# Optimization experiments

Hardware: AMD Instinct MI355X
Metric: run time of the kernel (lower is better)

## Reference

```python
import math
import jax, jax.numpy as jnp
import numpy as np

GRAIN = 300   # bilinear / grain dim (gpconv output channels)
PAD = 4       # explicit zero padding before each conv1d / conv2d
POOL = 40     # adaptive pool target (mf_model_pool_dim)

def conv1d_k2(x, w, b):
    # x: [B, L, Cin], w: [Cout, Cin, 2] -> [B, L-1, Cout]
    return (jnp.einsum('blc,oc->blo', x[:, :-1], w[:, :, 0])
            + jnp.einsum('blc,oc->blo', x[:, 1:], w[:, :, 1]) + b)

def kmax_last(x, k):
    # torch-style k-max pooling: top-k values along last axis, original order kept
    idx = jnp.sort(jax.lax.top_k(x, k)[1], axis=-1)
    return jnp.take_along_axis(x, idx, axis=-1)

def kmax_len(x, k):
    # k-max pooling over the length axis (axis=1) of [B, L, C]
    return jnp.swapaxes(kmax_last(jnp.swapaxes(x, 1, 2), k), 1, 2)

def adaptive_max_1d(x, out, axis):
    # torch AdaptiveMaxPool semantics along one axis; windows precomputed statically
    L = x.shape[axis]
    r = np.arange(out)
    starts = (r * L) // out
    ends = -((-(r + 1) * L) // out)
    maxw = int((ends - starts).max())
    off = starts[:, None] + np.arange(maxw)[None, :]
    mask = jnp.asarray(off < ends[:, None])
    idxs = np.minimum(off, L - 1)
    xm = jnp.moveaxis(x, axis, -1)
    g = jnp.where(mask, xm[..., idxs], -jnp.inf)
    return jnp.moveaxis(g.max(-1), -1, axis)

def conv2d_p4(x, w, b):
    y = jax.lax.conv_general_dilated(x, w, (1, 1), [(PAD, PAD), (PAD, PAD)],
                                     dimension_numbers=('NCHW', 'OIHW', 'NCHW'))
    return y + b[None, :, None, None]

def gp_tower(x, w1, b1, w2, b2, w3, b3, k1, k2):
    # multigranular conv tower: zero-pad(4) -> conv1d(k=2) -> tanh -> k-max pool
    g0 = kmax_last(x, GRAIN)                      # [B, L, 300]
    def block(z, w, b, k):
        z = jnp.pad(z, ((0, 0), (PAD, PAD), (0, 0)))
        return kmax_len(jnp.tanh(conv1d_k2(z, w, b)), k)
    p1 = block(x, w1, b1, k1)                     # [B, k1, 300]
    p2 = block(p1, w2, b2, k2)                    # [B, k2, 300]
    p3 = block(p2, w3, b3, 1)                     # [B, 1, 300]
    return jnp.concatenate([g0, p1, p2, p3], axis=1)

def _forward(query, pos_doc, neg_docs, qw1, qb1, qw2, qb2, qw3, qb3,
             dw1, db1, dw2, db2, dw3, db3, bw, bb,
             mw1, mb1, mw2, mb2, mw3, mb3, lw, lb):
    B, Lq, _ = query.shape
    S, _, Ld, _ = neg_docs.shape
    kq1, kq2 = max(4, math.ceil(2 * Lq / 3)), max(4, math.ceil(Lq / 3))
    kd1, kd2 = max(4, math.ceil(2 * Ld / 3)), max(4, math.ceil(Ld / 3))
    qg = gp_tower(query, qw1, qb1, qw2, qb2, qw3, qb3, kq1, kq2)   # [B, Nq, 300]
    docs = jnp.concatenate([pos_doc[None], neg_docs], 0).reshape((S + 1) * B, Ld, -1)
    dg = gp_tower(docs, dw1, db1, dw2, db2, dw3, db3, kd1, kd2)    # [(S+1)B, Nd, 300]
    Nq, Nd = qg.shape[1], dg.shape[1]
    dg = dg.reshape(S + 1, B, Nd, GRAIN)
    # batched bilinear matching + sigmoid (replaces the O(Nq*Nd) per-pair loop)
    qt = jnp.einsum('bqd,de->bqe', qg, bw)
    M = jax.nn.sigmoid(jnp.einsum('bqe,sbje->sbqj', qt, dg) + bb[0])
    M = M.reshape((S + 1) * B, Nq, Nd)
    x = adaptive_max_1d(adaptive_max_1d(M, POOL, 1), POOL, 2)[:, None]  # [N,1,40,40]
    for w, b in ((mw1, mb1), (mw2, mb2), (mw3, mb3)):
        x = jax.nn.sigmoid(conv2d_p4(x, w, b))
        x = adaptive_max_1d(adaptive_max_1d(x, POOL, 2), POOL, 3)
        x = x.max(axis=1, keepdims=True)          # k-max(k=1) over channels
    feat = x[:, 0]                                # [N, 40, 40]
    h = jax.nn.sigmoid(jnp.einsum('nij,j->ni', feat, lw[0]) + lb[0])
    s = jax.nn.sigmoid(h @ lw[0] + lb[0])
    return s.reshape(S + 1, B)                    # row 0 = pos-doc scores

def setup_inputs():
    ks = jax.random.split(jax.random.key(0), 26)
    def n(i, shape, s=0.05):
        return jax.random.normal(ks[i], shape, dtype=jnp.float32) * s
    return dict(
        query=jax.random.normal(ks[0], (16, 239, 1024), dtype=jnp.float32),
        pos_doc=jax.random.normal(ks[1], (16, 479, 1024), dtype=jnp.float32),
        neg_docs=jax.random.normal(ks[2], (4, 16, 479, 1024), dtype=jnp.float32),
        qw1=n(3, (300, 1024, 2)), qb1=n(4, (300,)),
        qw2=n(5, (300, 300, 2)), qb2=n(6, (300,)),
        qw3=n(7, (300, 300, 2)), qb3=n(8, (300,)),
        dw1=n(9, (300, 1024, 2)), db1=n(10, (300,)),
        dw2=n(11, (300, 300, 2)), db2=n(12, (300,)),
        dw3=n(13, (300, 300, 2)), db3=n(14, (300,)),
        bw=n(15, (300, 300)), bb=n(16, (1,)),
        mw1=n(17, (50, 1, 2, 2)), mb1=n(18, (50,)),
        mw2=n(19, (50, 1, 2, 2)), mb2=n(20, (50,)),
        mw3=n(21, (50, 1, 2, 2)), mb3=n(22, (50,)),
        lw=n(23, (1, 40)), lb=n(24, (1,)),
    )

def reference(query, pos_doc, neg_docs, qw1, qb1, qw2, qb2, qw3, qb3,
              dw1, db1, dw2, db2, dw3, db3, bw, bb,
              mw1, mb1, mw2, mb2, mw3, mb3, lw, lb):
    return _forward(query, pos_doc, neg_docs, qw1, qb1, qw2, qb2, qw3, qb3,
                    dw1, db1, dw2, db2, dw3, db3, bw, bb,
                    mw1, mb1, mw2, mb2, mw3, mb3, lw, lb)
```

## Files before the change

kernel.cpp:

```cpp
#include <hip/hip_runtime.h>
#include <hip/hip_bf16.h>
#include <math.h>

typedef unsigned long long ull;
typedef unsigned int uint;
typedef unsigned short ushort_t;

typedef short bf16x8 __attribute__((ext_vector_type(8)));
typedef float floatx4 __attribute__((ext_vector_type(4)));

__device__ inline ushort_t f2b(float f) {
    uint u = __float_as_uint(f);
    u = u + 0x7fffu + ((u >> 16) & 1u);
    return (ushort_t)(u >> 16);
}

__device__ inline uint kmap16(ushort_t u) {
    return (u & 0x8000u) ? (uint)((~u) & 0xFFFFu) : (uint)(u | 0x8000u);
}
__device__ inline ushort_t kinv16(uint k) {
    return (k & 0x8000u) ? (ushort_t)(k ^ 0x8000u) : (ushort_t)((~k) & 0xFFFFu);
}

__device__ inline void async_copy16(const void* g, void* l) {
    __builtin_amdgcn_global_load_lds(
        (const __attribute__((address_space(1))) void*)g,
        (__attribute__((address_space(3))) void*)l, 16, 0, 0);
}

__global__ void prep_w2_kernel(const float* __restrict__ w, ushort_t* __restrict__ Wb,
                               int C, int CP) {
    int CHn = CP / 32;
    int total = CHn * 2 * 20 * 512;
    for (int i = blockIdx.x * blockDim.x + threadIdx.x; i < total;
         i += gridDim.x * blockDim.x) {
        int e = i & 7;
        int lane = (i >> 3) & 63;
        int rest = i >> 9;
        int g = rest % 20;
        int tc = rest / 20;
        int t = tc & 1, c = tc >> 1;
        int o = g * 16 + (lane & 15);
        int ch = c * 32 + (lane >> 4) * 8 + e;
        float v = (o < 300 && ch < C) ? w[((size_t)o * C + ch) * 2 + t] : 0.f;
        Wb[i] = f2b(v);
    }
}

__global__ void prep_bw_kernel(const float* __restrict__ bw, ushort_t* __restrict__ bwb) {
    int i = blockIdx.x * 256 + threadIdx.x;
    if (i >= 320 * 320) return;
    int e = i / 320, d = i - e * 320;
    bwb[i] = (e < 300 && d < 300) ? f2b(bw[d * 300 + e]) : (ushort_t)0;
}

__global__ __launch_bounds__(256) void x_pad_bf16_kernel(
    const float* __restrict__ src, const float* __restrict__ src2, int split_n,
    long long s_nstr, int Lin, ushort_t* __restrict__ dst, int rows)
{
    int r = blockIdx.x, n = blockIdx.y;
    const float* sp = (split_n > 0 && n >= split_n)
                          ? src2 + (size_t)(n - split_n) * s_nstr
                          : src + (size_t)n * s_nstr;
    int g = r - 4;
    ushort_t* dp = dst + ((size_t)n * rows + r) * 1024;
    int c = threadIdx.x * 4;
    ushort4 o = {0, 0, 0, 0};
    if (g >= 0 && g < Lin) {
        float4 v = *(const float4*)&sp[(size_t)g * 1024 + c];
        o.x = f2b(v.x); o.y = f2b(v.y); o.z = f2b(v.z); o.w = f2b(v.w);
    }
    *(ushort4*)&dp[c] = o;
}

template <int CP>
__global__ __launch_bounds__(256, 2) void conv_wave_kernel(
    const ushort_t* __restrict__ xq, long long xq_nstr,
    const ushort_t* __restrict__ xd, long long xd_nstr,
    const ushort_t* __restrict__ Wq, const ushort_t* __restrict__ Wd,
    const float* __restrict__ bq, const float* __restrict__ bd,
    int Lout_q, int Lout_d, int mtiles_q, int mtiles_d,
    ushort_t* __restrict__ yt)
{
    constexpr int CH = CP / 32;
    constexpr int SLOT = 129 * 64;
    __shared__ char Abuf[4][2][SLOT];

    int tid = threadIdx.x, wid = tid >> 6, lane = tid & 63;
    int u = blockIdx.x * 4 + wid;
    int md5 = mtiles_d * 5, DOCU = md5 * 80;

    const ushort_t* x; const ushort_t* W; const float* bias;
    int Lout, mt, nt, ng;
    if (u < DOCU) {
        int nd = u / md5, r = u - nd * md5;
        mt = r / 5; nt = r - mt * 5;
        x = xd + (size_t)nd * xd_nstr; W = Wd; bias = bd; Lout = Lout_d;
        ng = 16 + nd;
    } else {
        int v = u - DOCU, mq5 = mtiles_q * 5;
        int nq = v / mq5, r = v - nq * mq5;
        mt = r / 5; nt = r - mt * 5;
        x = xq + (size_t)nq * xq_nstr; W = Wq; bias = bq; Lout = Lout_q;
        ng = nq;
    }
    int l0 = mt * 128;
    int lrow = lane & 15, quad = lane >> 4;

    const ushort_t* gMain = x + (size_t)(l0 + (lane >> 2)) * CP
                              + ((lane & 3) ^ ((lane >> 3) & 3)) * 8;
    const ushort_t* gXtra = x + (size_t)(l0 + 128) * CP + lane * 8;

    const ushort_t* Bw = W + (size_t)(nt * 4) * 512 + lane * 8;

    int baseA[2];
#pragma unroll
    for (int t = 0; t < 2; t++) {
        int rr = lrow + t;
        baseA[t] = rr * 64 + ((quad ^ ((rr >> 1) & 3)) << 4);
    }

    floatx4 acc[8][4];
#pragma unroll
    for (int i = 0; i < 8; i++)
#pragma unroll
        for (int j = 0; j < 4; j++) acc[i][j] = (floatx4){0.f, 0.f, 0.f, 0.f};

    char* lb0 = &Abuf[wid][0][0];

    auto STAGE = [&](int cc, int slot) {
        char* lb = lb0 + slot * SLOT;
        const ushort_t* gs = gMain + cc * 32;
#pragma unroll
        for (int g = 0; g < 8; g++)
            async_copy16(gs + (size_t)(g * 16) * CP, lb + g * 1024);
        if (lane < 4) async_copy16(gXtra + cc * 32, lb + 8192);
    };
    auto LOADB = [&](bf16x8 (&bf)[2][4], int cc) {
#pragma unroll
        for (int t = 0; t < 2; t++)
#pragma unroll
            for (int ns = 0; ns < 4; ns++)
                bf[t][ns] = *(const bf16x8*)(Bw + (size_t)((cc * 2 + t) * 20 + ns) * 512);
    };
    auto COMPUTE = [&](bf16x8 (&bf)[2][4], int slot) {
        const char* ab = lb0 + slot * SLOT;
        __builtin_amdgcn_s_setprio(1);
#pragma unroll
        for (int t = 0; t < 2; t++) {
#pragma unroll
            for (int ms = 0; ms < 8; ms++) {
                bf16x8 af = *(const bf16x8*)(ab + baseA[t] + ms * 1024);
#pragma unroll
                for (int ns = 0; ns < 4; ns++)
                    acc[ms][ns] = __builtin_amdgcn_mfma_f32_16x16x32_bf16(
                        af, bf[t][ns], acc[ms][ns], 0, 0, 0);
            }
        }
        __builtin_amdgcn_s_setprio(0);
    };
    auto WAITA = [&]() {
        asm volatile("s_waitcnt vmcnt(8)" ::: "memory");
        __builtin_amdgcn_sched_barrier(0);
    };

    bf16x8 bA[2][4], bB[2][4];

    STAGE(0, 0);
    __builtin_amdgcn_sched_barrier(0x38F);
    LOADB(bA, 0);

    for (int c = 0; c < CH; c += 2) {
        WAITA();
        if (c + 1 < CH) {
            STAGE(c + 1, (c + 1) & 1);
            __builtin_amdgcn_sched_barrier(0x38F);
            LOADB(bB, c + 1);
            __builtin_amdgcn_sched_barrier(0x38F);
        }
        COMPUTE(bA, c & 1);

        WAITA();
        if (c + 2 < CH) {
            STAGE(c + 2, (c + 2) & 1);
            __builtin_amdgcn_sched_barrier(0x38F);
            LOADB(bA, c + 2);
            __builtin_amdgcn_sched_barrier(0x38F);
        }
        COMPUTE(bB, (c + 1) & 1);
    }

    ushort_t* yp = yt + (size_t)ng * (320 * 488);
#pragma unroll
    for (int ns = 0; ns < 4; ns++) {
        int o = nt * 64 + ns * 16 + lrow;
        if (o >= 300) continue;
        float bo = bias[o];
        ushort_t* orow = yp + (size_t)o * 488;
#pragma unroll
        for (int ms = 0; ms < 8; ms++) {
            int l = l0 + ms * 16 + quad * 4;
            if (l + 3 < Lout) {
                ushort4 v;
                v.x = f2b(tanhf(acc[ms][ns][0] + bo));
                v.y = f2b(tanhf(acc[ms][ns][1] + bo));
                v.z = f2b(tanhf(acc[ms][ns][2] + bo));
                v.w = f2b(tanhf(acc[ms][ns][3] + bo));
                *(ushort4*)&orow[l] = v;
            } else {
#pragma unroll
                for (int r = 0; r < 4; r++)
                    if (l + r < Lout) orow[l + r] = f2b(tanhf(acc[ms][ns][r] + bo));
            }
        }
    }
}

__global__ __launch_bounds__(256) void topk_g0_kernel(
    const ushort_t* __restrict__ src, int CC, long long s_n,
    ushort_t* __restrict__ out, long long o_n, long long o_c)
{
    __shared__ uint hist[4][257];

    int tid = threadIdx.x, wid = tid >> 6, lane = tid & 63;
    int row = blockIdx.x * 4 + wid;
    int n = row / CC, c = row - n * CC;
    const ushort_t* sp = src + (size_t)n * s_n + (size_t)c * 1024;

    const uint* sp32 = (const uint*)(sp + (size_t)lane * 16);
    uint pk[8];
    {
        uint4 va = *(const uint4*)sp32;
        uint4 vb = *(const uint4*)(sp32 + 4);
        pk[0] = va.x; pk[1] = va.y; pk[2] = va.z; pk[3] = va.w;
        pk[4] = vb.x; pk[5] = vb.y; pk[6] = vb.z; pk[7] = vb.w;
    }
    uint key[16];
#pragma unroll
    for (int i = 0; i < 8; i++) {
        uint w = pk[i];
        uint s = w & 0x80008000u;
        w ^= 0x80008000u | ((s >> 15) * 0x7fffu);
        key[2 * i] = w & 0xffffu;
        key[2 * i + 1] = w >> 16;
    }

    uint* hg = hist[wid];
    uint rem = 300, bsel = 0, T = 0;

#pragma unroll
    for (int round = 0; round < 2; round++) {
#pragma unroll
        for (int t = 0; t < 4; t++) hg[lane + t * 64] = 0;
        __builtin_amdgcn_sched_barrier(0);
        if (round == 0) {
#pragma unroll
            for (int e = 0; e < 16; e++) atomicAdd(&hg[key[e] >> 8], 1u);
        } else {
#pragma unroll
            for (int e = 0; e < 16; e++)
                if ((key[e] >> 8) == bsel) atomicAdd(&hg[key[e] & 255u], 1u);
        }
        __builtin_amdgcn_sched_barrier(0);
        uint hv[4], Sr = 0;
#pragma unroll
        for (int t = 0; t < 4; t++) { hv[t] = hg[lane * 4 + t]; Sr += hv[t]; }
        uint suf = Sr;
#pragma unroll
        for (int off = 1; off < 64; off <<= 1) {
            uint u = __shfl_down(suf, off);
            if (lane + off < 64) suf += u;
        }
        uint acc = suf - Sr;
        uint found = 0;
#pragma unroll
        for (int t = 3; t >= 0; t--) {
            uint h = hv[t];
            if (!found && acc < rem && acc + h >= rem)
                found = ((uint)(lane * 4 + t) << 16) | (rem - acc);
            acc += h;
        }
#pragma unroll
        for (int off = 1; off < 64; off <<= 1) found |= __shfl_xor(found, off);
        if (round == 0) {
            bsel = found >> 16;
            rem = found & 0xffffu;
        } else {
            T = (bsel << 8) | (found >> 16);
            rem = found & 0xffffu;
        }
        __builtin_amdgcn_sched_barrier(0);
    }

    uint gtc = 0, eqc = 0;
#pragma unroll
    for (int e = 0; e < 16; e++) {
        gtc += (key[e] > T) ? 1u : 0u;
        eqc += (key[e] == T) ? 1u : 0u;
    }
    uint pack = (gtc << 16) | eqc, incl = pack;
#pragma unroll
    for (int off = 1; off < 64; off <<= 1) {
        uint u = __shfl_up(incl, off);
        if (lane >= off) incl += u;
    }
    uint excl = incl - pack;
    uint gt_b = excl >> 16, eq_b = excl & 0xffffu;

    ushort_t* dp = out + (size_t)n * o_n + (size_t)c * o_c;
#pragma unroll
    for (int e = 0; e < 16; e++) {
        uint kk = key[e];
        if (kk > T) {
            uint pos = gt_b + (eq_b < rem ? eq_b : rem);
            dp[pos] = kinv16(kk);
            gt_b++;
        } else if (kk == T) {
            if (eq_b < rem) dp[gt_b + eq_b] = kinv16(kk);
            eq_b++;
        }
    }
}

__global__ __launch_bounds__(256) void topk_cols_kernel(
    const ushort_t* __restrict__ yt2,
    int Lq, int Ld, int kq, int kd,
    ushort_t* __restrict__ qg, int qoff,
    ushort_t* __restrict__ dg, int doff,
    ushort_t* __restrict__ pq, long long pq_nstr,
    ushort_t* __restrict__ pd, long long pd_nstr)
{
    __shared__ __align__(16) ushort_t xin[32][488];
    __shared__ __align__(16) uint hist[32 * 257];
    ushort_t* otile = (ushort_t*)hist;

    int cg = blockIdx.x, n = blockIdx.y;
    int c0 = cg * 32;
    bool isq = (n < 16);
    int L = isq ? Lq : Ld;
    int k = isq ? kq : kd;
    int nd = isq ? n : n - 16;
    int tid = threadIdx.x;

    const ushort_t* src = yt2 + (size_t)n * (320 * 488) + (size_t)c0 * 488;
    for (int i = tid; i < 32 * 61; i += 256) {
        int j = i / 61, s = i - j * 61;
        *(uint4*)&xin[j][s * 8] = *(const uint4*)&src[(size_t)j * 488 + s * 8];
    }
    __syncthreads();

    int g = tid >> 3, r = tid & 7;
    uint* hg = &hist[g * 257];
    bool cval = (c0 + g) < 300;
    int S = (L + 7) >> 3;
    int llo = r * S, lhi = llo + S;
    if (lhi > L) lhi = L;
    if (llo > L) llo = L;

    uint rem = (uint)k;
    uint bsel = 0;
    uint Tt = 0;

#pragma unroll
    for (int round = 0; round < 2; round++) {
        for (int t = r; t < 256; t += 8) hg[t] = 0;
        for (int l = llo; l < lhi; l++) {
            uint key = cval ? kmap16(xin[g][l]) : 0x8000u;
            if (round == 0)
                atomicAdd(&hg[key >> 8], 1u);
            else if ((key >> 8) == bsel)
                atomicAdd(&hg[key & 255u], 1u);
        }
        uint hv[32];
        uint Sr = 0;
        int b0 = r * 32;
#pragma unroll
        for (int t = 0; t < 32; t++) { hv[t] = hg[b0 + t]; Sr += hv[t]; }
        uint suf = Sr;
#pragma unroll
        for (int off = 1; off < 8; off <<= 1) {
            uint u = __shfl_down(suf, off);
            if (r + off < 8) suf += u;
        }
        uint acc = suf - Sr;
        uint found = 0;
#pragma unroll
        for (int t = 31; t >= 0; t--) {
            uint h = hv[t];
            if (!found && acc < rem && acc + h >= rem)
                found = ((uint)(b0 + t) << 16) | (rem - acc);
            acc += h;
        }
#pragma unroll
        for (int off = 1; off < 8; off <<= 1) found |= __shfl_xor(found, off);
        if (round == 0) {
            bsel = found >> 16;
            rem = found & 0xffffu;
        } else {
            Tt = (bsel << 8) | (found >> 16);
            rem = found & 0xffffu;
        }
    }

    uint gtc = 0, eqc = 0;
    for (int l = llo; l < lhi; l++) {
        uint key = cval ? kmap16(xin[g][l]) : 0x8000u;
        gtc += (key > Tt) ? 1u : 0u;
        eqc += (key == Tt) ? 1u : 0u;
    }
    uint pack = (gtc << 16) | eqc, incl = pack;
#pragma unroll
    for (int off = 1; off < 8; off <<= 1) {
        uint u = __shfl_up(incl, off);
        if (r >= off) incl += u;
    }
    uint excl = incl - pack;
    uint gt_b = excl >> 16, eq_b = excl & 0xffffu;

    __syncthreads();

    for (int l = llo; l < lhi; l++) {
        uint key = cval ? kmap16(xin[g][l]) : 0x8000u;
        if (key > Tt) {
            uint pos = gt_b + (eq_b < rem ? eq_b : rem);
            otile[pos * 32 + g] = kinv16(key);
            gt_b++;
        } else if (key == Tt) {
            if (eq_b < rem) otile[(gt_b + eq_b) * 32 + g] = kinv16(key);
            eq_b++;
        }
    }
    __syncthreads();

    ushort_t* d1 = isq ? qg + ((size_t)nd * 480 + qoff) * 320 + c0
                       : dg + ((size_t)nd * 960 + doff) * 320 + c0;
    ushort_t* d2 = 0;
    if (isq) { if (pq) d2 = pq + (size_t)nd * pq_nstr + 4 * 320 + c0; }
    else     { if (pd) d2 = pd + (size_t)nd * pd_nstr + 4 * 320 + c0; }

    for (int i = tid; i < k * 8; i += 256) {
        int p = i >> 3, s = i & 7;
        ushort4 v = *(ushort4*)&otile[p * 32 + s * 4];
        *(ushort4*)&d1[(size_t)p * 320 + s * 4] = v;
        if (d2) *(ushort4*)&d2[(size_t)p * 320 + s * 4] = v;
    }
}

__global__ __launch_bounds__(256) void qt_mfma_kernel(
    const ushort_t* __restrict__ qgb, const ushort_t* __restrict__ bwb,
    ushort_t* __restrict__ qtb)
{
    int mt = blockIdx.x, b = blockIdx.y;
    int tid = threadIdx.x, wid = tid >> 6, lane = tid & 63;
    int wn = wid * 80, lrow = lane & 15, quad = lane >> 4;

    const ushort_t* A = qgb + ((size_t)b * 480 + mt * 48 + lrow) * 320 + quad * 8;
    const ushort_t* B = bwb + (size_t)(wn + lrow) * 320 + quad * 8;

    floatx4 acc[3][5];
#pragma unroll
    for (int i = 0; i < 3; i++)
#pragma unroll
        for (int j = 0; j < 5; j++) acc[i][j] = (floatx4){0.f, 0.f, 0.f, 0.f};

#pragma unroll 5
    for (int c0 = 0; c0 < 320; c0 += 32) {
        bf16x8 af[3], bfr[5];
#pragma unroll
        for (int ms = 0; ms < 3; ms++)
            af[ms] = *(const bf16x8*)&A[(size_t)(ms * 16) * 320 + c0];
#pragma unroll
        for (int ns = 0; ns < 5; ns++)
            bfr[ns] = *(const bf16x8*)&B[(size_t)(ns * 16) * 320 + c0];
#pragma unroll
        for (int ms = 0; ms < 3; ms++)
#pragma unroll
            for (int ns = 0; ns < 5; ns++)
                acc[ms][ns] = __builtin_amdgcn_mfma_f32_16x16x32_bf16(
                    af[ms], bfr[ns], acc[ms][ns], 0, 0, 0);
    }

    ushort_t* out = qtb + ((size_t)b * 480 + mt * 48) * 320;
#pragma unroll
    for (int ms = 0; ms < 3; ms++)
#pragma unroll
        for (int ns = 0; ns < 5; ns++)
#pragma unroll
            for (int r = 0; r < 4; r++)
                out[(size_t)(ms * 16 + quad * 4 + r) * 320 + wn + ns * 16 + lrow] =
                    f2b(acc[ms][ns][r]);
}

__global__ __launch_bounds__(256) void mpool_mfma_kernel(
    const ushort_t* __restrict__ qtb16, const ushort_t* __restrict__ dgb16,
    const float* __restrict__ bb, float* __restrict__ mp)
{
    __shared__ float pool[2 * 12 * 192];

    int jb = blockIdx.x;
    int qb = blockIdx.y;
    int n  = blockIdx.z;
    int b  = n & 15;

    int tid = threadIdx.x;
    int wid = tid >> 6, lane = tid & 63;
    int wm2 = wid >> 1;
    int wm = wm2 * 48, wn = (wid & 1) * 96;
    int lrow = lane & 15, quad = lane >> 4;

    const ushort_t* Abase = qtb16 + ((size_t)b * 480 + qb * 96 + wm) * 320 + quad * 8;
    const ushort_t* Bbase = dgb16 + ((size_t)n * 960 + jb * 192 + wn) * 320 + quad * 8;

    floatx4 acc[3][6];
#pragma unroll
    for (int i = 0; i < 3; i++)
#pragma unroll
        for (int j = 0; j < 6; j++) acc[i][j] = (floatx4){0.f, 0.f, 0.f, 0.f};

#pragma unroll 2
    for (int c0 = 0; c0 < 320; c0 += 32) {
        bf16x8 af[3], bfr[6];
#pragma unroll
        for (int mt = 0; mt < 3; mt++)
            af[mt] = *(const bf16x8*)&Abase[(size_t)(mt * 16 + lrow) * 320 + c0];
#pragma unroll
        for (int nt = 0; nt < 6; nt++)
            bfr[nt] = *(const bf16x8*)&Bbase[(size_t)(nt * 16 + lrow) * 320 + c0];
#pragma unroll
        for (int mt = 0; mt < 3; mt++)
#pragma unroll
            for (int nt = 0; nt < 6; nt++)
                acc[mt][nt] = __builtin_amdgcn_mfma_f32_16x16x32_bf16(
                    af[mt], bfr[nt], acc[mt][nt], 0, 0, 0);
    }

#pragma unroll
    for (int mt = 0; mt < 3; mt++) {
        int g = mt * 4 + quad;
#pragma unroll
        for (int nt = 0; nt < 6; nt++) {
            floatx4 a = acc[mt][nt];
            float rm = fmaxf(fmaxf(a[0], a[1]), fmaxf(a[2], a[3]));
            pool[(wm2 * 12 + g) * 192 + wn + nt * 16 + lrow] = rm;
        }
    }
    __syncthreads();

    if (tid < 64) {
        int qw = tid >> 3, jw = tid & 7;
        int slab = qw >> 2, w = qw & 3;
        float m = -INFINITY;
        const float* pp = &pool[(slab * 12 + w * 3) * 192 + jw * 24];
        for (int g = 0; g < 3; g++)
            for (int cc = 0; cc < 24; cc++)
                m = fmaxf(m, pp[g * 192 + cc]);
        float sig = 1.f / (1.f + expf(-(m + bb[0])));
        mp[(size_t)n * 1600 + (size_t)(qb * 8 + qw) * 40 + (jb * 8 + jw)] = sig;
    }
}

#define OCG 10
__global__ __launch_bounds__(256) void convblock_atomic_kernel(
    const float* __restrict__ X, const float* __restrict__ w,
    const float* __restrict__ bias, uint* __restrict__ Y)
{
    __shared__ float xp[48 * 48];
    __shared__ float ys[47 * 47];
    __shared__ float t1[40 * 47];
    __shared__ float outacc[1600];

    int n = blockIdx.x, t = threadIdx.x;
    int oc0 = blockIdx.y * OCG;
    const float* xn = X + (size_t)n * 1600;
    for (int i = t; i < 48 * 48; i += 256) {
        int r = i / 48, c = i - r * 48;
        int rr = r - 4, cc = c - 4;
        xp[i] = (rr >= 0 && rr < 40 && cc >= 0 && cc < 40) ? xn[rr * 40 + cc] : 0.f;
    }
    for (int i = t; i < 1600; i += 256) outacc[i] = 0.f;
    __syncthreads();

    for (int oc = oc0; oc < oc0 + OCG; oc++) {
        float w00 = w[oc * 4 + 0], w01 = w[oc * 4 + 1];
        float w10 = w[oc * 4 + 2], w11 = w[oc * 4 + 3];
        float bo = bias[oc];
        for (int i = t; i < 47 * 47; i += 256) {
            int r = i / 47, c = i - r * 47;
            float v = xp[r * 48 + c] * w00 + xp[r * 48 + c + 1] * w01
                    + xp[(r + 1) * 48 + c] * w10 + xp[(r + 1) * 48 + c + 1] * w11 + bo;
            ys[i] = 1.f / (1.f + expf(-v));
        }
        __syncthreads();
        for (int i = t; i < 40 * 47; i += 256) {
            int r = i / 47, c = i - r * 47;
            int s = (47 * r) / 40, e = (47 * (r + 1) + 39) / 40;
            float m = ys[s * 47 + c];
            for (int x = s + 1; x < e; x++) m = fmaxf(m, ys[x * 47 + c]);
            t1[i] = m;
        }
        __syncthreads();
        for (int i = t; i < 1600; i += 256) {
            int r = i / 40, c = i - r * 40;
            int s = (47 * c) / 40, e = (47 * (c + 1) + 39) / 40;
            float m = t1[r * 47 + s];
            for (int x = s + 1; x < e; x++) m = fmaxf(m, t1[r * 47 + x]);
            outacc[i] = fmaxf(outacc[i], m);
        }
        __syncthreads();
    }
    for (int i = t; i < 1600; i += 256)
        atomicMax(&Y[(size_t)n * 1600 + i], __float_as_uint(outacc[i]));
}

__global__ __launch_bounds__(64) void head_kernel(
    const float* __restrict__ feat, const float* __restrict__ lw,
    const float* __restrict__ lb, float* __restrict__ out)
{
    __shared__ float hs[40];
    int n = blockIdx.x, t = threadIdx.x;
    const float* f = feat + (size_t)n * 1600;
    if (t < 40) {
        float a = 0.f;
        for (int j = 0; j < 40; j++) a += f[t * 40 + j] * lw[j];
        hs[t] = 1.f / (1.f + expf(-(a + lb[0])));
    }
    __syncthreads();
    if (t == 0) {
        float a = 0.f;
        for (int i = 0; i < 40; i++) a += hs[i] * lw[i];
        out[n] = 1.f / (1.f + expf(-(a + lb[0])));
    }
}

extern "C" void kernel_launch(void* const* d_in, const int* in_sizes, int n_in,
                              void* d_out, int out_size, void* d_ws, size_t ws_size,
                              hipStream_t stream) {
    const float* query    = (const float*)d_in[0];
    const float* pos_doc  = (const float*)d_in[1];
    const float* neg_docs = (const float*)d_in[2];
    const float* qw1 = (const float*)d_in[3];  const float* qb1 = (const float*)d_in[4];
    const float* qw2 = (const float*)d_in[5];  const float* qb2 = (const float*)d_in[6];
    const float* qw3 = (const float*)d_in[7];  const float* qb3 = (const float*)d_in[8];
    const float* dw1 = (const float*)d_in[9];  const float* db1 = (const float*)d_in[10];
    const float* dw2 = (const float*)d_in[11]; const float* db2 = (const float*)d_in[12];
    const float* dw3 = (const float*)d_in[13]; const float* db3 = (const float*)d_in[14];
    const float* bw  = (const float*)d_in[15]; const float* bb  = (const float*)d_in[16];
    const float* mw1 = (const float*)d_in[17]; const float* mb1 = (const float*)d_in[18];
    const float* mw2 = (const float*)d_in[19]; const float* mb2 = (const float*)d_in[20];
    const float* mw3 = (const float*)d_in[21]; const float* mb3 = (const float*)d_in[22];
    const float* lw  = (const float*)d_in[23]; const float* lb  = (const float*)d_in[24];

    float* ws = (float*)d_ws;
    ushort_t* qw1b  = (ushort_t*)(ws + 0);
    ushort_t* qw2b  = (ushort_t*)(ws + 327680);
    ushort_t* qw3b  = (ushort_t*)(ws + 430080);
    ushort_t* dw1b  = (ushort_t*)(ws + 532480);
    ushort_t* dw2b  = (ushort_t*)(ws + 860160);
    ushort_t* dw3b  = (ushort_t*)(ws + 962560);
    ushort_t* bwb   = (ushort_t*)(ws + 1064960);
    ushort_t* qgb16 = (ushort_t*)(ws + 1116160);
    ushort_t* dgb16 = (ushort_t*)(ws + 2344960);
    ushort_t* yt    = (ushort_t*)(ws + 14632960);
    ushort_t* qxb   = (ushort_t*)(ws + 22128640);
    ushort_t* p1q   = (ushort_t*)(ws + 22128640);
    ushort_t* p2q   = (ushort_t*)(ws + 22640640);
    ushort_t* dxb   = (ushort_t*)(ws + 24291328);
    ushort_t* p1d   = (ushort_t*)(ws + 24291328);
    ushort_t* p2d   = (ushort_t*)(ws + 28899328);
    ushort_t* qtb16 = (ushort_t*)(ws + 31459328);
    float*    mp    = ws + 32688128;
    float*    ya    = ws + 32816128;
    float*    yb    = ws + 32944128;
    float*    yc    = ws + 33072128;

    prep_w2_kernel<<<1280, 256, 0, stream>>>(qw1, qw1b, 1024, 1024);
    prep_w2_kernel<<<400, 256, 0, stream>>>(qw2, qw2b, 300, 320);
    prep_w2_kernel<<<400, 256, 0, stream>>>(qw3, qw3b, 300, 320);
    prep_w2_kernel<<<1280, 256, 0, stream>>>(dw1, dw1b, 1024, 1024);
    prep_w2_kernel<<<400, 256, 0, stream>>>(dw2, dw2b, 300, 320);
    prep_w2_kernel<<<400, 256, 0, stream>>>(dw3, dw3b, 300, 320);
    prep_bw_kernel<<<400, 256, 0, stream>>>(bw, bwb);

    {
        dim3 g(264, 16);
        x_pad_bf16_kernel<<<g, 256, 0, stream>>>(query, nullptr, 0,
                                                 239LL * 1024, 239, qxb, 264);
    }
    {
        dim3 g(520, 80);
        x_pad_bf16_kernel<<<g, 256, 0, stream>>>(pos_doc, neg_docs, 16,
                                                 479LL * 1024, 479, dxb, 520);
    }

    topk_g0_kernel<<<(16 * 239) / 4, 256, 0, stream>>>(
        qxb + 4 * 1024, 239, 264LL * 1024, qgb16, 480LL * 320, 320);
    topk_g0_kernel<<<(80 * 479) / 4, 256, 0, stream>>>(
        dxb + 4 * 1024, 479, 520LL * 1024, dgb16, 960LL * 320, 320);

    conv_wave_kernel<1024><<<440, 256, 0, stream>>>(
        qxb, 264LL * 1024, dxb, 520LL * 1024,
        qw1b, dw1b, qb1, db1, 246, 486, 2, 4, yt);

    hipMemsetAsync(p1q, 0, 16 * 200 * 320 * 2, stream);
    hipMemsetAsync(p2q, 0, 16 * 104 * 320 * 2, stream);
    hipMemsetAsync(p1d, 0, (size_t)80 * 360 * 320 * 2, stream);
    hipMemsetAsync(p2d, 0, (size_t)80 * 200 * 320 * 2, stream);
    hipMemsetAsync(ya, 0, 80 * 1600 * 4, stream);
    hipMemsetAsync(yb, 0, 80 * 1600 * 4, stream);
    hipMemsetAsync(yc, 0, 80 * 1600 * 4, stream);

    {
        dim3 g(10, 96);
        topk_cols_kernel<<<g, 256, 0, stream>>>(
            yt, 246, 486, 160, 320,
            qgb16, 239, dgb16, 479,
            p1q, 200LL * 320, p1d, 360LL * 320);
    }

    conv_wave_kernel<320><<<340, 256, 0, stream>>>(
        p1q, 200LL * 320, p1d, 360LL * 320,
        qw2b, dw2b, qb2, db2, 167, 327, 2, 3, yt);

    {
        dim3 g(10, 96);
        topk_cols_kernel<<<g, 256, 0, stream>>>(
            yt, 167, 327, 80, 160,
            qgb16, 399, dgb16, 799,
            p2q, 104LL * 320, p2d, 200LL * 320);
    }

    conv_wave_kernel<320><<<220, 256, 0, stream>>>(
        p2q, 104LL * 320, p2d, 200LL * 320,
        qw3b, dw3b, qb3, db3, 87, 167, 1, 2, yt);

    {
        dim3 g(10, 96);
        topk_cols_kernel<<<g, 256, 0, stream>>>(
            yt, 87, 167, 1, 1,
            qgb16, 479, dgb16, 959,
            nullptr, 0, nullptr, 0);
    }

    {
        dim3 g(10, 16);
        qt_mfma_kernel<<<g, 256, 0, stream>>>(qgb16, bwb, qtb16);
    }
    {
        dim3 g(5, 5, 80);
        mpool_mfma_kernel<<<g, 256, 0, stream>>>(qtb16, dgb16, bb, mp);
    }

    {
        dim3 g(80, 5);
        convblock_atomic_kernel<<<g, 256, 0, stream>>>(mp, mw1, mb1, (uint*)ya);
        convblock_atomic_kernel<<<g, 256, 0, stream>>>(ya, mw2, mb2, (uint*)yb);
        convblock_atomic_kernel<<<g, 256, 0, stream>>>(yb, mw3, mb3, (uint*)yc);
    }
    head_kernel<<<80, 64, 0, stream>>>(yc, lw, lb, (float*)d_out);
}
```

Measured before the change: 1.112 ms.

## Add 64-row conv tile kernel with 3-stage pipeline for layers two and three

Adds a new conv kernel variant that computes 64-row M tiles per wave (instead of 128), uses a triple-buffered async LDS staging pipeline and allows 3 blocks per CU. Layers two and three now launch this variant with more tiles and blocks, while the original 128-row kernel is kept under a new name for the first layer. The aim is to raise parallelism and occupancy for the smaller later convolutions, which underfill the GPU. The cost is less reuse of each weight load across rows and more blocks to schedule.

After: 1.081 ms. 1.03x faster.

```diff
diff --git a/kernel.cpp b/kernel.cpp
--- a/kernel.cpp
+++ b/kernel.cpp
@@ -74,7 +74,137 @@
 }
 
 template <int CP>
-__global__ __launch_bounds__(256, 2) void conv_wave_kernel(
+__global__ __launch_bounds__(256, 3) void conv_wave_kernel(
+    const ushort_t* __restrict__ xq, long long xq_nstr,
+    const ushort_t* __restrict__ xd, long long xd_nstr,
+    const ushort_t* __restrict__ Wq, const ushort_t* __restrict__ Wd,
+    const float* __restrict__ bq, const float* __restrict__ bd,
+    int Lout_q, int Lout_d, int mtiles_q, int mtiles_d,
+    ushort_t* __restrict__ yt)
+{
+    constexpr int CH = CP / 32;
+    __shared__ char Abuf[4][3][4160];
+
+    int tid = threadIdx.x, wid = tid >> 6, lane = tid & 63;
+    int u = blockIdx.x * 4 + wid;
+    int md5 = mtiles_d * 5, DOCU = md5 * 80;
+
+    const ushort_t* x; const ushort_t* W; const float* bias;
+    int Lout, mt, nt, ng;
+    if (u < DOCU) {
+        int nd = u / md5, r = u - nd * md5;
+        mt = r / 5; nt = r - mt * 5;
+        x = xd + (size_t)nd * xd_nstr; W = Wd; bias = bd; Lout = Lout_d;
+        ng = 16 + nd;
+    } else {
+        int v = u - DOCU, mq5 = mtiles_q * 5;
+        int nq = v / mq5, r = v - nq * mq5;
+        mt = r / 5; nt = r - mt * 5;
+        x = xq + (size_t)nq * xq_nstr; W = Wq; bias = bq; Lout = Lout_q;
+        ng = nq;
+    }
+    int l0 = mt * 64;
+    int lrow = lane & 15, quad = lane >> 4;
+
+    const ushort_t* gMain = x + (size_t)(l0 + (lane >> 2)) * CP
+                              + ((lane & 3) ^ ((lane >> 3) & 3)) * 8;
+    const ushort_t* gXtra = x + (size_t)(l0 + 64) * CP + lane * 8;
+
+    const ushort_t* Bw = W + (size_t)(nt * 4) * 512 + lane * 8;
+
+    int offA[2][4];
+#pragma unroll
+    for (int t = 0; t < 2; t++)
+#pragma unroll
+        for (int ms = 0; ms < 4; ms++) {
+            int r = ms * 16 + lrow + t;
+            offA[t][ms] = r * 64 + ((quad ^ ((r >> 1) & 3)) << 4);
+        }
+
+    floatx4 acc[4][4];
+#pragma unroll
+    for (int i = 0; i < 4; i++)
+#pragma unroll
+        for (int j = 0; j < 4; j++) acc[i][j] = (floatx4){0.f, 0.f, 0.f, 0.f};
+
+    char* lb0 = &Abuf[wid][0][0];
+
+    auto STAGE = [&](int cc, int slot) {
+        char* lb = lb0 + slot * 4160;
+        const ushort_t* gs = gMain + cc * 32;
+        async_copy16(gs, lb);
+        async_copy16(gs + (size_t)16 * CP, lb + 1024);
+        async_copy16(gs + (size_t)32 * CP, lb + 2048);
+        async_copy16(gs + (size_t)48 * CP, lb + 3072);
+        if (lane < 4) async_copy16(gXtra + cc * 32, lb + 4096);
+    };
+
+    STAGE(0, 0);
+    STAGE(1, 1);
+
+    for (int c = 0; c < CH; c++) {
+        if (c == 0) asm volatile("s_waitcnt vmcnt(5)" ::: "memory");
+        else        asm volatile("s_waitcnt vmcnt(8)" ::: "memory");
+        __builtin_amdgcn_sched_barrier(0);
+
+        bf16x8 bf[2][4];
+#pragma unroll
+        for (int t = 0; t < 2; t++)
+#pragma unroll
+            for (int ns = 0; ns < 4; ns++)
+                bf[t][ns] = *(const bf16x8*)(Bw + (size_t)((c * 2 + t) * 20 + ns) * 512);
+        __builtin_amdgcn_sched_barrier(0x38F);
+
+        if (c + 2 < CH) STAGE(c + 2, (c + 2) % 3);
+
+        const char* ab = lb0 + (c % 3) * 4160;
+        __builtin_amdgcn_s_setprio(1);
+#pragma unroll
+        for (int t = 0; t < 2; t++) {
+            bf16x8 af[4];
+#pragma unroll
+            for (int ms = 0; ms < 4; ms++)
+                af[ms] = *(const bf16x8*)(ab + offA[t][ms]);
+#pragma unroll
+            for (int ms = 0; ms < 4; ms++)
+#pragma unroll
+                for (int ns = 0; ns < 4; ns++)
+                    acc[ms][ns] = __builtin_amdgcn_mfma_f32_16x16x32_bf16(
+                        af[ms], bf[t][ns], acc[ms][ns], 0, 0, 0);
+        }
+        __builtin_amdgcn_s_setprio(0);
+    }
+
+    ushort_t* yp = yt + (size_t)ng * (320 * 488);
+#pragma unroll
+    for (int ns = 0; ns < 4; ns++) {
+        int o = nt * 64 + ns * 16 + lrow;
+        if (o >= 300) continue;
+        float bo = bias[o];
+        ushort_t* orow = yp + (size_t)o * 488;
+#pragma unroll
+        for (int ms = 0; ms < 4; ms++) {
+            int l = l0 + ms * 16 + quad * 4;
+            if (l + 3 < Lout) {
+                ushort4 v;
+                v.x = f2b(tanhf(acc[ms][ns][0] + bo));
+                v.y = f2b(tanhf(acc[ms][ns][1] + bo));
+                v.z = f2b(tanhf(acc[ms][ns][2] + bo));
+                v.w = f2b(tanhf(acc[ms][ns][3] + bo));
+                *(ushort4*)&orow[l] = v;
+            } else {
+#pragma unroll
+                for (int r = 0; r < 4; r++)
+                    if (l + r < Lout) orow[l + r] = f2b(tanhf(acc[ms][ns][r] + bo));
+            }
+        }
+    }
+}
+
+template <int CP>
+__global__ __launch_bounds__(256)
+__attribute__((amdgpu_waves_per_eu(2, 2)))
+void conv_wave128_kernel(
     const ushort_t* __restrict__ xq, long long xq_nstr,
     const ushort_t* __restrict__ xd, long long xd_nstr,
     const ushort_t* __restrict__ Wq, const ushort_t* __restrict__ Wd,
@@ -697,7 +827,7 @@
     topk_g0_kernel<<<(80 * 479) / 4, 256, 0, stream>>>(
         dxb + 4 * 1024, 479, 520LL * 1024, dgb16, 960LL * 320, 320);
 
-    conv_wave_kernel<1024><<<440, 256, 0, stream>>>(
+    conv_wave128_kernel<1024><<<440, 256, 0, stream>>>(
         qxb, 264LL * 1024, dxb, 520LL * 1024,
         qw1b, dw1b, qb1, db1, 246, 486, 2, 4, yt);
 
@@ -717,9 +847,9 @@
             p1q, 200LL * 320, p1d, 360LL * 320);
     }
 
-    conv_wave_kernel<320><<<340, 256, 0, stream>>>(
+    conv_wave_kernel<320><<<660, 256, 0, stream>>>(
         p1q, 200LL * 320, p1d, 360LL * 320,
-        qw2b, dw2b, qb2, db2, 167, 327, 2, 3, yt);
+        qw2b, dw2b, qb2, db2, 167, 327, 3, 6, yt);
 
     {
         dim3 g(10, 96);
@@ -729,9 +859,9 @@
             p2q, 104LL * 320, p2d, 200LL * 320);
     }
 
-    conv_wave_kernel<320><<<220, 256, 0, stream>>>(
+    conv_wave_kernel<320><<<340, 256, 0, stream>>>(
         p2q, 104LL * 320, p2d, 200LL * 320,
-        qw3b, dw3b, qb3, db3, 87, 167, 1, 2, yt);
+        qw3b, dw3b, qb3, db3, 87, 167, 2, 3, yt);
 
     {
         dim3 g(10, 96);
```
